# Kernel optimization log

Measured on AMD Instinct MI355X. Metric: run time of the kernel, lower is better.

## Reference

```python
import jax, jax.numpy as jnp
import numpy as np

B, T, C = 512, 256, 384
HEAD_SIZE = 64

def setup_inputs() -> dict:
    key = jax.random.key(0)
    k1, k2, k3, k4 = jax.random.split(key, 4)
    x = jax.random.normal(k1, (B, T, C), dtype=jnp.float32)
    # nn.Linear(n_embed, head_size, bias=False) weights, stored as [C, head_size] for x @ W
    s = 1.0 / np.sqrt(C)
    Wk = jax.random.uniform(k2, (C, HEAD_SIZE), dtype=jnp.float32, minval=-s, maxval=s)
    Wq = jax.random.uniform(k3, (C, HEAD_SIZE), dtype=jnp.float32, minval=-s, maxval=s)
    Wv = jax.random.uniform(k4, (C, HEAD_SIZE), dtype=jnp.float32, minval=-s, maxval=s)
    return {"x": x, "Wk": Wk, "Wq": Wq, "Wv": Wv}

def reference(x, Wk, Wq, Wv):
    # Single causal self-attention head (eval mode: dropout is identity).
    Bx, Tx, Cx = x.shape
    k = jnp.einsum('btc,ch->bth', x, Wk)   # [B,T,H]
    q = jnp.einsum('btc,ch->bth', x, Wq)
    v = jnp.einsum('btc,ch->bth', x, Wv)
    # NOTE: original scales by C**-0.5 with C = input embed dim (384), not head_size.
    wei = jnp.einsum('bth,bsh->bts', q, k) * (Cx ** -0.5)  # [B,T,T]
    causal = jnp.tril(jnp.ones((Tx, Tx), dtype=bool))
    wei = jnp.where(causal, wei, -jnp.inf)
    wei = jax.nn.softmax(wei, axis=-1)
    out = jnp.einsum('bts,bsh->bth', wei, v)  # [B,T,H]
    return out
```

## Files before the change

kernel.cpp:

```cpp
#include <hip/hip_runtime.h>

typedef __attribute__((ext_vector_type(4))) float f32x4;
typedef __attribute__((ext_vector_type(8))) short short8;
typedef unsigned int u32;
typedef unsigned long long u64;
typedef unsigned short u16;

#define NB 512
#define TT 256
#define CC 384
#define HH 64

__device__ __forceinline__ u16 fbf(float f) {
    u32 u = __builtin_bit_cast(u32, f);
    u32 r = u + 0x7fffu + ((u >> 16) & 1u);
    return (u16)(r >> 16);
}

__device__ __forceinline__ f32x4 mfma16x16x32(short8 a, short8 b, f32x4 c) {
    return __builtin_amdgcn_mfma_f32_16x16x32_bf16(a, b, c, 0, 0, 0);
}

__global__ __launch_bounds__(256) void prep_w(const float* __restrict__ Wk,
                                              const float* __restrict__ Wq,
                                              const float* __restrict__ Wv,
                                              u16* __restrict__ WbT) {
    int t = blockIdx.x * 256 + threadIdx.x;
    if (t >= 144 * 64) return;
    int lane = t & 63;
    int fi = t >> 6;
    int mat = fi / 48;
    int kt = (fi >> 2) % 12;
    int nt = fi & 3;
    const float* W = (mat == 0) ? Wq : (mat == 1 ? Wk : Wv);
    float scale = (mat == 0) ? 0.05103103630798288f : 1.0f;
    int c0 = 32 * kt + 8 * (lane >> 4);
    int h = 16 * nt + (lane & 15);
#pragma unroll
    for (int j = 0; j < 8; ++j)
        WbT[(size_t)t * 8 + j] = fbf(W[(c0 + j) * HH + h] * scale);
}

__global__ __launch_bounds__(512) void attn_head(const float* __restrict__ x,
                                                 const u16* __restrict__ WbT,
                                                 float* __restrict__ out) {
    __shared__ __align__(16) u16 Klds[TT * HH];
    __shared__ __align__(16) u16 Vtlds[HH * TT];
    __shared__ __align__(16) u16 Pscr[8 * 32 * 64];

    const int tid = (int)threadIdx.x;
    const int lane = tid & 63;
    const int w = tid >> 6;
    const int c = lane & 15;
    const int g = lane >> 4;
    const int b = (int)blockIdx.x;
    const int m0 = 32 * w;

    char* kbase = (char*)Klds;
    char* vbase = (char*)Vtlds;
    char* sbase = (char*)(Pscr + w * 2048);

    f32x4 acc[3][2][4];
#pragma unroll
    for (int m = 0; m < 3; ++m)
#pragma unroll
        for (int tm = 0; tm < 2; ++tm)
#pragma unroll
            for (int nt = 0; nt < 4; ++nt)
                acc[m][tm][nt] = (f32x4){0.f, 0.f, 0.f, 0.f};

    const float* xb = x + (size_t)b * TT * CC;

    for (int kt = 0; kt < 12; ++kt) {
        short8 afr[2];
#pragma unroll
        for (int tm = 0; tm < 2; ++tm) {
            const float* p = xb + (size_t)(m0 + 16 * tm + c) * CC + 32 * kt + 8 * g;
            f32x4 f0 = *(const f32x4*)p;
            f32x4 f1 = *(const f32x4*)(p + 4);
            short8 a;
            a[0] = (short)fbf(f0[0]); a[1] = (short)fbf(f0[1]);
            a[2] = (short)fbf(f0[2]); a[3] = (short)fbf(f0[3]);
            a[4] = (short)fbf(f1[0]); a[5] = (short)fbf(f1[1]);
            a[6] = (short)fbf(f1[2]); a[7] = (short)fbf(f1[3]);
            afr[tm] = a;
        }
#pragma unroll
        for (int mat = 0; mat < 3; ++mat) {
#pragma unroll
            for (int nt = 0; nt < 4; ++nt) {
                short8 bfr = *(const short8*)(WbT + (size_t)(((mat * 12 + kt) * 4 + nt) * 64 + lane) * 8);
                acc[mat][0][nt] = mfma16x16x32(afr[0], bfr, acc[mat][0][nt]);
                acc[mat][1][nt] = mfma16x16x32(afr[1], bfr, acc[mat][1][nt]);
            }
        }
    }

#pragma unroll
    for (int tm = 0; tm < 2; ++tm)
#pragma unroll
        for (int nt = 0; nt < 4; ++nt)
#pragma unroll
            for (int r = 0; r < 4; ++r) {
                int q = 16 * tm + 4 * g + r;
                int hh = 16 * nt + c;
                *(u16*)(sbase + q * 128 + ((hh * 2) ^ ((q & 7) << 4))) = fbf(acc[0][tm][nt][r]);
            }
    short8 Qf[2][2];
#pragma unroll
    for (int tm = 0; tm < 2; ++tm)
#pragma unroll
        for (int kt = 0; kt < 2; ++kt) {
            int q = 16 * tm + c;
            Qf[tm][kt] = *(const short8*)(sbase + q * 128 + ((64 * kt + 16 * g) ^ ((q & 7) << 4)));
        }

#pragma unroll
    for (int tm = 0; tm < 2; ++tm)
#pragma unroll
        for (int nt = 0; nt < 4; ++nt) {
            int hh = 16 * nt + c;
#pragma unroll
            for (int r = 0; r < 4; ++r) {
                int s = m0 + 16 * tm + 4 * g + r;
                *(u16*)(kbase + s * 128 + ((hh * 2) ^ ((s & 7) << 4))) = fbf(acc[1][tm][nt][r]);
            }
            int sb4 = m0 + 16 * tm + 4 * g;
            u64 pk = (u64)fbf(acc[2][tm][nt][0]) | ((u64)fbf(acc[2][tm][nt][1]) << 16) |
                     ((u64)fbf(acc[2][tm][nt][2]) << 32) | ((u64)fbf(acc[2][tm][nt][3]) << 48);
            *(u64*)(vbase + hh * 512 + ((sb4 * 2) ^ ((hh & 7) << 4))) = pk;
        }

    __syncthreads();

    float m_run0 = -1e30f, m_run1 = -1e30f, l_run0 = 0.f, l_run1 = 0.f;
    f32x4 o[2][4];
#pragma unroll
    for (int tm = 0; tm < 2; ++tm)
#pragma unroll
        for (int ht = 0; ht < 4; ++ht)
            o[tm][ht] = (f32x4){0.f, 0.f, 0.f, 0.f};

    const int nch = (w >> 1) + 1;
    for (int ci = 0; ci < nch; ++ci) {
        const int s0 = 64 * ci;
        int stmax = (m0 + 31 - s0) >> 4;
        stmax = stmax > 3 ? 3 : stmax;

        f32x4 SS[4][2];
#pragma unroll
        for (int st = 0; st < 4; ++st) {
            SS[st][0] = (f32x4){0.f, 0.f, 0.f, 0.f};
            SS[st][1] = (f32x4){0.f, 0.f, 0.f, 0.f};
        }
#pragma unroll
        for (int kt = 0; kt < 2; ++kt) {
#pragma unroll
            for (int st = 0; st < 4; ++st) {
                if (st <= stmax) {
                    int s = s0 + 16 * st + c;
                    short8 kf = *(const short8*)(kbase + s * 128 + ((64 * kt + 16 * g) ^ ((s & 7) << 4)));
                    SS[st][0] = mfma16x16x32(kf, Qf[0][kt], SS[st][0]);
                    SS[st][1] = mfma16x16x32(kf, Qf[1][kt], SS[st][1]);
                }
            }
        }

        float mx0 = -1e30f, mx1 = -1e30f;
        const int qg0 = m0 + c, qg1 = m0 + 16 + c;
#pragma unroll
        for (int st = 0; st < 4; ++st) {
            if (st > stmax) continue;
#pragma unroll
            for (int r = 0; r < 4; ++r) {
                int sg = s0 + 16 * st + 4 * g + r;
                float v0 = SS[st][0][r], v1 = SS[st][1][r];
                v0 = (sg > qg0) ? -1e30f : v0;
                v1 = (sg > qg1) ? -1e30f : v1;
                SS[st][0][r] = v0; SS[st][1][r] = v1;
                mx0 = fmaxf(mx0, v0); mx1 = fmaxf(mx1, v1);
            }
        }
        mx0 = fmaxf(mx0, __shfl_xor(mx0, 16));
        mx0 = fmaxf(mx0, __shfl_xor(mx0, 32));
        mx1 = fmaxf(mx1, __shfl_xor(mx1, 16));
        mx1 = fmaxf(mx1, __shfl_xor(mx1, 32));

        float mn0 = fmaxf(m_run0, mx0), mn1 = fmaxf(m_run1, mx1);
        float fs0 = __expf(m_run0 - mn0), fs1 = __expf(m_run1 - mn1);
        m_run0 = mn0; m_run1 = mn1;

        float ls0 = 0.f, ls1 = 0.f;
#pragma unroll
        for (int st = 0; st < 4; ++st) {
            if (st > stmax) continue;
#pragma unroll
            for (int r = 0; r < 4; ++r) {
                float p0 = __expf(SS[st][0][r] - mn0);
                float p1 = __expf(SS[st][1][r] - mn1);
                SS[st][0][r] = p0; SS[st][1][r] = p1;
                ls0 += p0; ls1 += p1;
            }
        }
        ls0 += __shfl_xor(ls0, 16); ls0 += __shfl_xor(ls0, 32);
        ls1 += __shfl_xor(ls1, 16); ls1 += __shfl_xor(ls1, 32);
        l_run0 = l_run0 * fs0 + ls0;
        l_run1 = l_run1 * fs1 + ls1;

#pragma unroll
        for (int r = 0; r < 4; ++r) {
            float fr0 = __shfl(fs0, (g << 2) + r);
            float fr1 = __shfl(fs1, (g << 2) + r);
#pragma unroll
            for (int ht = 0; ht < 4; ++ht) {
                o[0][ht][r] *= fr0;
                o[1][ht][r] *= fr1;
            }
        }

#pragma unroll
        for (int st = 0; st < 4; ++st) {
            if (st > stmax) continue;
#pragma unroll
            for (int tm = 0; tm < 2; ++tm) {
                int ql = 16 * tm + c;
                u32 lo = (u32)fbf(SS[st][tm][0]) | ((u32)fbf(SS[st][tm][1]) << 16);
                u32 hi = (u32)fbf(SS[st][tm][2]) | ((u32)fbf(SS[st][tm][3]) << 16);
                *(u64*)(sbase + ql * 128 + ((32 * st + 8 * g) ^ ((ql & 7) << 4))) = (u64)lo | ((u64)hi << 32);
            }
        }

        const int ksmax = stmax >> 1;
#pragma unroll
        for (int ks = 0; ks < 2; ++ks) {
            if (ks > ksmax) continue;
            short8 Pf0 = *(const short8*)(sbase + c * 128 + ((64 * ks + 16 * g) ^ ((c & 7) << 4)));
            short8 Pf1 = *(const short8*)(sbase + (16 + c) * 128 + ((64 * ks + 16 * g) ^ ((c & 7) << 4)));
#pragma unroll
            for (int ht = 0; ht < 4; ++ht) {
                int hh = 16 * ht + c;
                short8 vf = *(const short8*)(vbase + hh * 512 + ((2 * s0 + 64 * ks + 16 * g) ^ ((hh & 7) << 4)));
                o[0][ht] = mfma16x16x32(Pf0, vf, o[0][ht]);
                o[1][ht] = mfma16x16x32(Pf1, vf, o[1][ht]);
            }
        }
    }

    float* ob = out + ((size_t)b * TT + m0) * HH;
    float ri0 = 1.f / l_run0, ri1 = 1.f / l_run1;
#pragma unroll
    for (int r = 0; r < 4; ++r) {
        float rr0 = __shfl(ri0, (g << 2) + r);
        float rr1 = __shfl(ri1, (g << 2) + r);
#pragma unroll
        for (int ht = 0; ht < 4; ++ht) {
            ob[(4 * g + r) * HH + 16 * ht + c] = o[0][ht][r] * rr0;
            ob[(16 + 4 * g + r) * HH + 16 * ht + c] = o[1][ht][r] * rr1;
        }
    }
}

extern "C" void kernel_launch(void* const* d_in, const int* in_sizes, int n_in,
                              void* d_out, int out_size, void* d_ws, size_t ws_size,
                              hipStream_t stream) {
    (void)in_sizes; (void)n_in; (void)out_size; (void)ws_size;
    const float* x = (const float*)d_in[0];
    const float* Wk = (const float*)d_in[1];
    const float* Wq = (const float*)d_in[2];
    const float* Wv = (const float*)d_in[3];
    u16* WbT = (u16*)d_ws;
    float* out = (float*)d_out;

    prep_w<<<36, 256, 0, stream>>>(Wk, Wq, Wv, WbT);
    attn_head<<<NB, 512, 0, stream>>>(x, WbT, out);
}
```

Measured before the change: 72.96 us.

## Balance causal work across waves and pass P through shuffles instead of LDS

Each wave now owns two 16-row query tiles from opposite ends of the sequence (16w and 240-16w), so the causal attention work is the same for every wave instead of growing with wave index. The per-wave P scratch buffer in LDS is removed. Q is staged through the K buffer, and the softmax probabilities are rearranged into MFMA operand layout with cross-lane shuffles. Float-to-bf16 packing now uses the v_cvt_pk_bf16_f32 instruction, and launch bounds request 4 blocks per CU, which adds register pressure and more shuffle instructions.

Result: slower. 175.2 us (+140.1%).

```diff
diff --git a/kernel.cpp b/kernel.cpp
--- a/kernel.cpp
+++ b/kernel.cpp
@@ -1,6 +1,7 @@
 #include <hip/hip_runtime.h>
 
 typedef __attribute__((ext_vector_type(4))) float f32x4;
+typedef __attribute__((ext_vector_type(4))) int i32x4;
 typedef __attribute__((ext_vector_type(8))) short short8;
 typedef unsigned int u32;
 typedef unsigned long long u64;
@@ -15,6 +16,12 @@
     u32 u = __builtin_bit_cast(u32, f);
     u32 r = u + 0x7fffu + ((u >> 16) & 1u);
     return (u16)(r >> 16);
+}
+
+__device__ __forceinline__ u32 cvtpk(float lo, float hi) {
+    u32 r;
+    asm("v_cvt_pk_bf16_f32 %0, %1, %2" : "=v"(r) : "v"(lo), "v"(hi));
+    return r;
 }
 
 __device__ __forceinline__ f32x4 mfma16x16x32(short8 a, short8 b, f32x4 c) {
@@ -41,12 +48,11 @@
         WbT[(size_t)t * 8 + j] = fbf(W[(c0 + j) * HH + h] * scale);
 }
 
-__global__ __launch_bounds__(512) void attn_head(const float* __restrict__ x,
-                                                 const u16* __restrict__ WbT,
-                                                 float* __restrict__ out) {
+__global__ __launch_bounds__(512, 4) void attn_head(const float* __restrict__ x,
+                                                    const u16* __restrict__ WbT,
+                                                    float* __restrict__ out) {
     __shared__ __align__(16) u16 Klds[TT * HH];
     __shared__ __align__(16) u16 Vtlds[HH * TT];
-    __shared__ __align__(16) u16 Pscr[8 * 32 * 64];
 
     const int tid = (int)threadIdx.x;
     const int lane = tid & 63;
@@ -54,208 +60,251 @@
     const int c = lane & 15;
     const int g = lane >> 4;
     const int b = (int)blockIdx.x;
-    const int m0 = 32 * w;
+    const int grow0 = 16 * w;
+    const int grow1 = 240 - 16 * w;
 
     char* kbase = (char*)Klds;
     char* vbase = (char*)Vtlds;
-    char* sbase = (char*)(Pscr + w * 2048);
-
-    f32x4 acc[3][2][4];
-#pragma unroll
-    for (int m = 0; m < 3; ++m)
-#pragma unroll
-        for (int tm = 0; tm < 2; ++tm)
+    const float* xb = x + (size_t)b * TT * CC;
+
+    short8 Qf[2][2];
+
+#pragma unroll
+    for (int tm = 0; tm < 2; ++tm) {
+        const int gr = (tm == 0) ? grow0 : grow1;
+        f32x4 acc[3][4];
+#pragma unroll
+        for (int m = 0; m < 3; ++m)
 #pragma unroll
             for (int nt = 0; nt < 4; ++nt)
-                acc[m][tm][nt] = (f32x4){0.f, 0.f, 0.f, 0.f};
-
-    const float* xb = x + (size_t)b * TT * CC;
-
-    for (int kt = 0; kt < 12; ++kt) {
-        short8 afr[2];
-#pragma unroll
-        for (int tm = 0; tm < 2; ++tm) {
-            const float* p = xb + (size_t)(m0 + 16 * tm + c) * CC + 32 * kt + 8 * g;
+                acc[m][nt] = (f32x4){0.f, 0.f, 0.f, 0.f};
+
+        for (int kt = 0; kt < 12; ++kt) {
+            const float* p = xb + (size_t)(gr + c) * CC + 32 * kt + 8 * g;
             f32x4 f0 = *(const f32x4*)p;
             f32x4 f1 = *(const f32x4*)(p + 4);
-            short8 a;
-            a[0] = (short)fbf(f0[0]); a[1] = (short)fbf(f0[1]);
-            a[2] = (short)fbf(f0[2]); a[3] = (short)fbf(f0[3]);
-            a[4] = (short)fbf(f1[0]); a[5] = (short)fbf(f1[1]);
-            a[6] = (short)fbf(f1[2]); a[7] = (short)fbf(f1[3]);
-            afr[tm] = a;
-        }
-#pragma unroll
-        for (int mat = 0; mat < 3; ++mat) {
-#pragma unroll
-            for (int nt = 0; nt < 4; ++nt) {
-                short8 bfr = *(const short8*)(WbT + (size_t)(((mat * 12 + kt) * 4 + nt) * 64 + lane) * 8);
-                acc[mat][0][nt] = mfma16x16x32(afr[0], bfr, acc[mat][0][nt]);
-                acc[mat][1][nt] = mfma16x16x32(afr[1], bfr, acc[mat][1][nt]);
-            }
-        }
-    }
-
-#pragma unroll
-    for (int tm = 0; tm < 2; ++tm)
+            i32x4 aw = {(int)cvtpk(f0[0], f0[1]), (int)cvtpk(f0[2], f0[3]),
+                        (int)cvtpk(f1[0], f1[1]), (int)cvtpk(f1[2], f1[3])};
+            short8 afr = __builtin_bit_cast(short8, aw);
+#pragma unroll
+            for (int mat = 0; mat < 3; ++mat)
+#pragma unroll
+                for (int nt = 0; nt < 4; ++nt) {
+                    short8 bfr = *(const short8*)(WbT + (size_t)(((mat * 12 + kt) * 4 + nt) * 64 + lane) * 8);
+                    acc[mat][nt] = mfma16x16x32(afr, bfr, acc[mat][nt]);
+                }
+        }
+
 #pragma unroll
         for (int nt = 0; nt < 4; ++nt)
 #pragma unroll
             for (int r = 0; r < 4; ++r) {
-                int q = 16 * tm + 4 * g + r;
+                int q = gr + 4 * g + r;
                 int hh = 16 * nt + c;
-                *(u16*)(sbase + q * 128 + ((hh * 2) ^ ((q & 7) << 4))) = fbf(acc[0][tm][nt][r]);
-            }
-    short8 Qf[2][2];
-#pragma unroll
-    for (int tm = 0; tm < 2; ++tm)
+                *(u16*)(kbase + q * 128 + ((hh * 2) ^ ((q & 7) << 4))) = fbf(acc[0][nt][r]);
+            }
 #pragma unroll
         for (int kt = 0; kt < 2; ++kt) {
-            int q = 16 * tm + c;
-            Qf[tm][kt] = *(const short8*)(sbase + q * 128 + ((64 * kt + 16 * g) ^ ((q & 7) << 4)));
-        }
-
-#pragma unroll
-    for (int tm = 0; tm < 2; ++tm)
+            int q = gr + c;
+            Qf[tm][kt] = *(const short8*)(kbase + q * 128 + ((64 * kt + 16 * g) ^ ((q & 7) << 4)));
+        }
+
 #pragma unroll
         for (int nt = 0; nt < 4; ++nt) {
             int hh = 16 * nt + c;
 #pragma unroll
             for (int r = 0; r < 4; ++r) {
-                int s = m0 + 16 * tm + 4 * g + r;
-                *(u16*)(kbase + s * 128 + ((hh * 2) ^ ((s & 7) << 4))) = fbf(acc[1][tm][nt][r]);
-            }
-            int sb4 = m0 + 16 * tm + 4 * g;
-            u64 pk = (u64)fbf(acc[2][tm][nt][0]) | ((u64)fbf(acc[2][tm][nt][1]) << 16) |
-                     ((u64)fbf(acc[2][tm][nt][2]) << 32) | ((u64)fbf(acc[2][tm][nt][3]) << 48);
-            *(u64*)(vbase + hh * 512 + ((sb4 * 2) ^ ((hh & 7) << 4))) = pk;
-        }
+                int s = gr + 4 * g + r;
+                *(u16*)(kbase + s * 128 + ((hh * 2) ^ ((s & 7) << 4))) = fbf(acc[1][nt][r]);
+            }
+            int sb4 = gr + 4 * g;
+            u64 pkv = (u64)cvtpk(acc[2][nt][0], acc[2][nt][1]) |
+                      ((u64)cvtpk(acc[2][nt][2], acc[2][nt][3]) << 32);
+            *(u64*)(vbase + hh * 512 + ((sb4 * 2) ^ ((hh & 7) << 4))) = pkv;
+        }
+    }
 
     __syncthreads();
 
     float m_run0 = -1e30f, m_run1 = -1e30f, l_run0 = 0.f, l_run1 = 0.f;
-    f32x4 o[2][4];
-#pragma unroll
-    for (int tm = 0; tm < 2; ++tm)
-#pragma unroll
-        for (int ht = 0; ht < 4; ++ht)
-            o[tm][ht] = (f32x4){0.f, 0.f, 0.f, 0.f};
-
-    const int nch = (w >> 1) + 1;
-    for (int ci = 0; ci < nch; ++ci) {
+    f32x4 o0[4], o1[4];
+#pragma unroll
+    for (int ht = 0; ht < 4; ++ht) {
+        o0[ht] = (f32x4){0.f, 0.f, 0.f, 0.f};
+        o1[ht] = (f32x4){0.f, 0.f, 0.f, 0.f};
+    }
+
+    const int lastc0 = (grow0 + 15) >> 6;
+    const int lastc1 = (grow1 + 15) >> 6;
+    const int srcLo = c + ((lane & 16) << 1);
+    const int srcHi = srcLo + 16;
+    const bool hiHalf = (lane >= 32);
+
+    for (int ci = 0; ci <= lastc1; ++ci) {
         const int s0 = 64 * ci;
-        int stmax = (m0 + 31 - s0) >> 4;
-        stmax = stmax > 3 ? 3 : stmax;
-
-        f32x4 SS[4][2];
+        const bool act0 = (ci <= lastc0);
+        const int stmax0 = act0 ? min(3, (grow0 + 15 - s0) >> 4) : -1;
+        const int stmax1 = min(3, (grow1 + 15 - s0) >> 4);
+        const int stmaxU = max(stmax0, stmax1);
+
+        f32x4 SS0[4], SS1[4];
 #pragma unroll
         for (int st = 0; st < 4; ++st) {
-            SS[st][0] = (f32x4){0.f, 0.f, 0.f, 0.f};
-            SS[st][1] = (f32x4){0.f, 0.f, 0.f, 0.f};
+            SS0[st] = (f32x4){0.f, 0.f, 0.f, 0.f};
+            SS1[st] = (f32x4){0.f, 0.f, 0.f, 0.f};
         }
 #pragma unroll
         for (int kt = 0; kt < 2; ++kt) {
 #pragma unroll
             for (int st = 0; st < 4; ++st) {
-                if (st <= stmax) {
+                if (st <= stmaxU) {
                     int s = s0 + 16 * st + c;
                     short8 kf = *(const short8*)(kbase + s * 128 + ((64 * kt + 16 * g) ^ ((s & 7) << 4)));
-                    SS[st][0] = mfma16x16x32(kf, Qf[0][kt], SS[st][0]);
-                    SS[st][1] = mfma16x16x32(kf, Qf[1][kt], SS[st][1]);
+                    if (st <= stmax0) SS0[st] = mfma16x16x32(kf, Qf[0][kt], SS0[st]);
+                    if (st <= stmax1) SS1[st] = mfma16x16x32(kf, Qf[1][kt], SS1[st]);
                 }
             }
         }
 
         float mx0 = -1e30f, mx1 = -1e30f;
-        const int qg0 = m0 + c, qg1 = m0 + 16 + c;
+        const int qg0 = grow0 + c, qg1 = grow1 + c;
 #pragma unroll
         for (int st = 0; st < 4; ++st) {
-            if (st > stmax) continue;
 #pragma unroll
             for (int r = 0; r < 4; ++r) {
                 int sg = s0 + 16 * st + 4 * g + r;
-                float v0 = SS[st][0][r], v1 = SS[st][1][r];
-                v0 = (sg > qg0) ? -1e30f : v0;
-                v1 = (sg > qg1) ? -1e30f : v1;
-                SS[st][0][r] = v0; SS[st][1][r] = v1;
-                mx0 = fmaxf(mx0, v0); mx1 = fmaxf(mx1, v1);
-            }
-        }
-        mx0 = fmaxf(mx0, __shfl_xor(mx0, 16));
-        mx0 = fmaxf(mx0, __shfl_xor(mx0, 32));
+                if (st <= stmax0) {
+                    float v = (sg > qg0) ? -1e30f : SS0[st][r];
+                    SS0[st][r] = v;
+                    mx0 = fmaxf(mx0, v);
+                }
+                if (st <= stmax1) {
+                    float v = (sg > qg1) ? -1e30f : SS1[st][r];
+                    SS1[st][r] = v;
+                    mx1 = fmaxf(mx1, v);
+                }
+            }
+        }
+        if (act0) {
+            mx0 = fmaxf(mx0, __shfl_xor(mx0, 16));
+            mx0 = fmaxf(mx0, __shfl_xor(mx0, 32));
+        }
         mx1 = fmaxf(mx1, __shfl_xor(mx1, 16));
         mx1 = fmaxf(mx1, __shfl_xor(mx1, 32));
 
-        float mn0 = fmaxf(m_run0, mx0), mn1 = fmaxf(m_run1, mx1);
-        float fs0 = __expf(m_run0 - mn0), fs1 = __expf(m_run1 - mn1);
-        m_run0 = mn0; m_run1 = mn1;
+        float fs0 = 1.f, fs1;
+        if (act0) {
+            float mn0 = fmaxf(m_run0, mx0);
+            fs0 = __expf(m_run0 - mn0);
+            m_run0 = mn0;
+        }
+        {
+            float mn1 = fmaxf(m_run1, mx1);
+            fs1 = __expf(m_run1 - mn1);
+            m_run1 = mn1;
+        }
 
         float ls0 = 0.f, ls1 = 0.f;
 #pragma unroll
         for (int st = 0; st < 4; ++st) {
-            if (st > stmax) continue;
 #pragma unroll
             for (int r = 0; r < 4; ++r) {
-                float p0 = __expf(SS[st][0][r] - mn0);
-                float p1 = __expf(SS[st][1][r] - mn1);
-                SS[st][0][r] = p0; SS[st][1][r] = p1;
-                ls0 += p0; ls1 += p1;
-            }
-        }
-        ls0 += __shfl_xor(ls0, 16); ls0 += __shfl_xor(ls0, 32);
-        ls1 += __shfl_xor(ls1, 16); ls1 += __shfl_xor(ls1, 32);
-        l_run0 = l_run0 * fs0 + ls0;
+                if (st <= stmax0) {
+                    float p = __expf(SS0[st][r] - m_run0);
+                    SS0[st][r] = p;
+                    ls0 += p;
+                }
+                if (st <= stmax1) {
+                    float p = __expf(SS1[st][r] - m_run1);
+                    SS1[st][r] = p;
+                    ls1 += p;
+                }
+            }
+        }
+        if (act0) {
+            ls0 += __shfl_xor(ls0, 16);
+            ls0 += __shfl_xor(ls0, 32);
+            l_run0 = l_run0 * fs0 + ls0;
+        }
+        ls1 += __shfl_xor(ls1, 16);
+        ls1 += __shfl_xor(ls1, 32);
         l_run1 = l_run1 * fs1 + ls1;
 
 #pragma unroll
         for (int r = 0; r < 4; ++r) {
-            float fr0 = __shfl(fs0, (g << 2) + r);
-            float fr1 = __shfl(fs1, (g << 2) + r);
+            float fr0 = __shfl(fs0, 4 * g + r);
+            float fr1 = __shfl(fs1, 4 * g + r);
 #pragma unroll
             for (int ht = 0; ht < 4; ++ht) {
-                o[0][ht][r] *= fr0;
-                o[1][ht][r] *= fr1;
-            }
-        }
-
+                if (act0) o0[ht][r] *= fr0;
+                o1[ht][r] *= fr1;
+            }
+        }
+
+        u32 pk0[4][2], pk1[4][2];
 #pragma unroll
         for (int st = 0; st < 4; ++st) {
-            if (st > stmax) continue;
-#pragma unroll
-            for (int tm = 0; tm < 2; ++tm) {
-                int ql = 16 * tm + c;
-                u32 lo = (u32)fbf(SS[st][tm][0]) | ((u32)fbf(SS[st][tm][1]) << 16);
-                u32 hi = (u32)fbf(SS[st][tm][2]) | ((u32)fbf(SS[st][tm][3]) << 16);
-                *(u64*)(sbase + ql * 128 + ((32 * st + 8 * g) ^ ((ql & 7) << 4))) = (u64)lo | ((u64)hi << 32);
-            }
-        }
-
-        const int ksmax = stmax >> 1;
+            pk0[st][0] = cvtpk(SS0[st][0], SS0[st][1]);
+            pk0[st][1] = cvtpk(SS0[st][2], SS0[st][3]);
+            pk1[st][0] = cvtpk(SS1[st][0], SS1[st][1]);
+            pk1[st][1] = cvtpk(SS1[st][2], SS1[st][3]);
+        }
+
+        const int ksmax0 = stmax0 >> 1;
+        const int ksmax1 = stmax1 >> 1;
 #pragma unroll
         for (int ks = 0; ks < 2; ++ks) {
-            if (ks > ksmax) continue;
-            short8 Pf0 = *(const short8*)(sbase + c * 128 + ((64 * ks + 16 * g) ^ ((c & 7) << 4)));
-            short8 Pf1 = *(const short8*)(sbase + (16 + c) * 128 + ((64 * ks + 16 * g) ^ ((c & 7) << 4)));
+            const bool u0 = (ks <= ksmax0);
+            const bool u1 = (ks <= ksmax1);
+            if (!(u0 || u1)) continue;
+            short8 Pf0, Pf1;
+            if (u0) {
+                u32 a0 = (u32)__shfl((int)pk0[2 * ks][0], srcLo);
+                u32 b0 = (u32)__shfl((int)pk0[2 * ks + 1][0], srcLo);
+                u32 a1 = (u32)__shfl((int)pk0[2 * ks][1], srcLo);
+                u32 b1 = (u32)__shfl((int)pk0[2 * ks + 1][1], srcLo);
+                u32 a2 = (u32)__shfl((int)pk0[2 * ks][0], srcHi);
+                u32 b2 = (u32)__shfl((int)pk0[2 * ks + 1][0], srcHi);
+                u32 a3 = (u32)__shfl((int)pk0[2 * ks][1], srcHi);
+                u32 b3 = (u32)__shfl((int)pk0[2 * ks + 1][1], srcHi);
+                i32x4 t = {(int)(hiHalf ? b0 : a0), (int)(hiHalf ? b1 : a1),
+                           (int)(hiHalf ? b2 : a2), (int)(hiHalf ? b3 : a3)};
+                Pf0 = __builtin_bit_cast(short8, t);
+            }
+            if (u1) {
+                u32 a0 = (u32)__shfl((int)pk1[2 * ks][0], srcLo);
+                u32 b0 = (u32)__shfl((int)pk1[2 * ks + 1][0], srcLo);
+                u32 a1 = (u32)__shfl((int)pk1[2 * ks][1], srcLo);
+                u32 b1 = (u32)__shfl((int)pk1[2 * ks + 1][1], srcLo);
+                u32 a2 = (u32)__shfl((int)pk1[2 * ks][0], srcHi);
+                u32 b2 = (u32)__shfl((int)pk1[2 * ks + 1][0], srcHi);
+                u32 a3 = (u32)__shfl((int)pk1[2 * ks][1], srcHi);
+                u32 b3 = (u32)__shfl((int)pk1[2 * ks + 1][1], srcHi);
+                i32x4 t = {(int)(hiHalf ? b0 : a0), (int)(hiHalf ? b1 : a1),
+                           (int)(hiHalf ? b2 : a2), (int)(hiHalf ? b3 : a3)};
+                Pf1 = __builtin_bit_cast(short8, t);
+            }
 #pragma unroll
             for (int ht = 0; ht < 4; ++ht) {
                 int hh = 16 * ht + c;
                 short8 vf = *(const short8*)(vbase + hh * 512 + ((2 * s0 + 64 * ks + 16 * g) ^ ((hh & 7) << 4)));
-                o[0][ht] = mfma16x16x32(Pf0, vf, o[0][ht]);
-                o[1][ht] = mfma16x16x32(Pf1, vf, o[1][ht]);
+                if (u0) o0[ht] = mfma16x16x32(Pf0, vf, o0[ht]);
+                if (u1) o1[ht] = mfma16x16x32(Pf1, vf, o1[ht]);
             }
         }
     }
 
-    float* ob = out + ((size_t)b * TT + m0) * HH;
     float ri0 = 1.f / l_run0, ri1 = 1.f / l_run1;
+    float* ob0 = out + ((size_t)b * TT + grow0) * HH;
+    float* ob1 = out + ((size_t)b * TT + grow1) * HH;
 #pragma unroll
     for (int r = 0; r < 4; ++r) {
-        float rr0 = __shfl(ri0, (g << 2) + r);
-        float rr1 = __shfl(ri1, (g << 2) + r);
+        float rr0 = __shfl(ri0, 4 * g + r);
+        float rr1 = __shfl(ri1, 4 * g + r);
 #pragma unroll
         for (int ht = 0; ht < 4; ++ht) {
-            ob[(4 * g + r) * HH + 16 * ht + c] = o[0][ht][r] * rr0;
-            ob[(16 + 4 * g + r) * HH + 16 * ht + c] = o[1][ht][r] * rr1;
+            ob0[(4 * g + r) * HH + 16 * ht + c] = o0[ht][r] * rr0;
+            ob1[(4 * g + r) * HH + 16 * ht + c] = o1[ht][r] * rr1;
         }
     }
 }
```

## Balance causal work across waves with paired row tiles and hardware bf16 packing

Applied to the files above, without the earlier changes.

Each wave now owns two 16-row query tiles taken from opposite ends of the sequence (16w and 240-16w), so every wave does about the same amount of causal attention work. Before, waves owning later rows did far more chunks than waves owning early rows. The projection and attention loops now handle one tile at a time, which lowers register pressure; launch bounds ask for 4 blocks per CU. Other changes: Q is staged through K's LDS slot before K overwrites it, the scratch buffer is halved, and fp32-to-bf16 conversion uses v_cvt_pk_bf16_f32. Masking is skipped for chunks that need none, and the first-chunk rescale is skipped.

New measurement: 129.2 us. +77.1%, slower.

```diff
diff --git a/kernel.cpp b/kernel.cpp
--- a/kernel.cpp
+++ b/kernel.cpp
@@ -1,6 +1,7 @@
 #include <hip/hip_runtime.h>
 
 typedef __attribute__((ext_vector_type(4))) float f32x4;
+typedef __attribute__((ext_vector_type(4))) int i32x4;
 typedef __attribute__((ext_vector_type(8))) short short8;
 typedef unsigned int u32;
 typedef unsigned long long u64;
@@ -15,6 +16,12 @@
     u32 u = __builtin_bit_cast(u32, f);
     u32 r = u + 0x7fffu + ((u >> 16) & 1u);
     return (u16)(r >> 16);
+}
+
+__device__ __forceinline__ u32 cvtpk(float lo, float hi) {
+    u32 r;
+    asm("v_cvt_pk_bf16_f32 %0, %1, %2" : "=v"(r) : "v"(lo), "v"(hi));
+    return r;
 }
 
 __device__ __forceinline__ f32x4 mfma16x16x32(short8 a, short8 b, f32x4 c) {
@@ -41,12 +48,12 @@
         WbT[(size_t)t * 8 + j] = fbf(W[(c0 + j) * HH + h] * scale);
 }
 
-__global__ __launch_bounds__(512) void attn_head(const float* __restrict__ x,
-                                                 const u16* __restrict__ WbT,
-                                                 float* __restrict__ out) {
+__global__ __launch_bounds__(512, 4) void attn_head(const float* __restrict__ x,
+                                                    const u16* __restrict__ WbT,
+                                                    float* __restrict__ out) {
     __shared__ __align__(16) u16 Klds[TT * HH];
     __shared__ __align__(16) u16 Vtlds[HH * TT];
-    __shared__ __align__(16) u16 Pscr[8 * 32 * 64];
+    __shared__ __align__(16) u16 Pscr[8 * 16 * 64];
 
     const int tid = (int)threadIdx.x;
     const int lane = tid & 63;
@@ -54,208 +61,182 @@
     const int c = lane & 15;
     const int g = lane >> 4;
     const int b = (int)blockIdx.x;
-    const int m0 = 32 * w;
 
     char* kbase = (char*)Klds;
     char* vbase = (char*)Vtlds;
-    char* sbase = (char*)(Pscr + w * 2048);
-
-    f32x4 acc[3][2][4];
-#pragma unroll
-    for (int m = 0; m < 3; ++m)
-#pragma unroll
-        for (int tm = 0; tm < 2; ++tm)
+    char* sbase = (char*)(Pscr + w * 1024);
+    const float* xb = x + (size_t)b * TT * CC;
+
+    short8 Qf[2][2];
+
+#pragma unroll
+    for (int tm = 0; tm < 2; ++tm) {
+        const int gr = (tm == 0) ? 16 * w : 240 - 16 * w;
+        f32x4 acc[3][4];
+#pragma unroll
+        for (int m = 0; m < 3; ++m)
 #pragma unroll
             for (int nt = 0; nt < 4; ++nt)
-                acc[m][tm][nt] = (f32x4){0.f, 0.f, 0.f, 0.f};
-
-    const float* xb = x + (size_t)b * TT * CC;
-
-    for (int kt = 0; kt < 12; ++kt) {
-        short8 afr[2];
-#pragma unroll
-        for (int tm = 0; tm < 2; ++tm) {
-            const float* p = xb + (size_t)(m0 + 16 * tm + c) * CC + 32 * kt + 8 * g;
-            f32x4 f0 = *(const f32x4*)p;
-            f32x4 f1 = *(const f32x4*)(p + 4);
-            short8 a;
-            a[0] = (short)fbf(f0[0]); a[1] = (short)fbf(f0[1]);
-            a[2] = (short)fbf(f0[2]); a[3] = (short)fbf(f0[3]);
-            a[4] = (short)fbf(f1[0]); a[5] = (short)fbf(f1[1]);
-            a[6] = (short)fbf(f1[2]); a[7] = (short)fbf(f1[3]);
-            afr[tm] = a;
-        }
-#pragma unroll
-        for (int mat = 0; mat < 3; ++mat) {
-#pragma unroll
-            for (int nt = 0; nt < 4; ++nt) {
-                short8 bfr = *(const short8*)(WbT + (size_t)(((mat * 12 + kt) * 4 + nt) * 64 + lane) * 8);
-                acc[mat][0][nt] = mfma16x16x32(afr[0], bfr, acc[mat][0][nt]);
-                acc[mat][1][nt] = mfma16x16x32(afr[1], bfr, acc[mat][1][nt]);
+                acc[m][nt] = (f32x4){0.f, 0.f, 0.f, 0.f};
+
+        const float* prow = xb + (size_t)(gr + c) * CC + 8 * g;
+#pragma unroll
+        for (int kt = 0; kt < 12; ++kt) {
+            f32x4 f0 = *(const f32x4*)(prow + 32 * kt);
+            f32x4 f1 = *(const f32x4*)(prow + 32 * kt + 4);
+            i32x4 aw = {(int)cvtpk(f0[0], f0[1]), (int)cvtpk(f0[2], f0[3]),
+                        (int)cvtpk(f1[0], f1[1]), (int)cvtpk(f1[2], f1[3])};
+            short8 afr = __builtin_bit_cast(short8, aw);
+#pragma unroll
+            for (int mat = 0; mat < 3; ++mat)
+#pragma unroll
+                for (int nt = 0; nt < 4; ++nt) {
+                    short8 bfr = *(const short8*)(WbT + (size_t)(((mat * 12 + kt) * 4 + nt) * 64 + lane) * 8);
+                    acc[mat][nt] = mfma16x16x32(afr, bfr, acc[mat][nt]);
+                }
+        }
+
+#pragma unroll
+        for (int nt = 0; nt < 4; ++nt)
+#pragma unroll
+            for (int r = 0; r < 4; ++r) {
+                int q = gr + 4 * g + r;
+                int hh = 16 * nt + c;
+                *(u16*)(kbase + q * 128 + ((hh * 2) ^ ((q & 7) << 4))) = fbf(acc[0][nt][r]);
             }
-        }
-    }
-
-#pragma unroll
-    for (int tm = 0; tm < 2; ++tm)
-#pragma unroll
-        for (int nt = 0; nt < 4; ++nt)
-#pragma unroll
-            for (int r = 0; r < 4; ++r) {
-                int q = 16 * tm + 4 * g + r;
-                int hh = 16 * nt + c;
-                *(u16*)(sbase + q * 128 + ((hh * 2) ^ ((q & 7) << 4))) = fbf(acc[0][tm][nt][r]);
-            }
-    short8 Qf[2][2];
-#pragma unroll
-    for (int tm = 0; tm < 2; ++tm)
 #pragma unroll
         for (int kt = 0; kt < 2; ++kt) {
-            int q = 16 * tm + c;
-            Qf[tm][kt] = *(const short8*)(sbase + q * 128 + ((64 * kt + 16 * g) ^ ((q & 7) << 4)));
-        }
-
-#pragma unroll
-    for (int tm = 0; tm < 2; ++tm)
+            int q = gr + c;
+            Qf[tm][kt] = *(const short8*)(kbase + q * 128 + ((64 * kt + 16 * g) ^ ((q & 7) << 4)));
+        }
+
 #pragma unroll
         for (int nt = 0; nt < 4; ++nt) {
             int hh = 16 * nt + c;
 #pragma unroll
             for (int r = 0; r < 4; ++r) {
-                int s = m0 + 16 * tm + 4 * g + r;
-                *(u16*)(kbase + s * 128 + ((hh * 2) ^ ((s & 7) << 4))) = fbf(acc[1][tm][nt][r]);
+                int s = gr + 4 * g + r;
+                *(u16*)(kbase + s * 128 + ((hh * 2) ^ ((s & 7) << 4))) = fbf(acc[1][nt][r]);
             }
-            int sb4 = m0 + 16 * tm + 4 * g;
-            u64 pk = (u64)fbf(acc[2][tm][nt][0]) | ((u64)fbf(acc[2][tm][nt][1]) << 16) |
-                     ((u64)fbf(acc[2][tm][nt][2]) << 32) | ((u64)fbf(acc[2][tm][nt][3]) << 48);
-            *(u64*)(vbase + hh * 512 + ((sb4 * 2) ^ ((hh & 7) << 4))) = pk;
-        }
+            int sb4 = gr + 4 * g;
+            u64 pkv = (u64)cvtpk(acc[2][nt][0], acc[2][nt][1]) |
+                      ((u64)cvtpk(acc[2][nt][2], acc[2][nt][3]) << 32);
+            *(u64*)(vbase + hh * 512 + ((sb4 * 2) ^ ((hh & 7) << 4))) = pkv;
+        }
+    }
 
     __syncthreads();
 
-    float m_run0 = -1e30f, m_run1 = -1e30f, l_run0 = 0.f, l_run1 = 0.f;
-    f32x4 o[2][4];
-#pragma unroll
-    for (int tm = 0; tm < 2; ++tm)
+#pragma unroll
+    for (int tm = 0; tm < 2; ++tm) {
+        const int gr = (tm == 0) ? 16 * w : 240 - 16 * w;
+        const int lastc = (gr + 15) >> 6;
+        const int qg = gr + c;
+
+        float m_run = -1e30f, l_run = 0.f;
+        f32x4 o[4];
 #pragma unroll
         for (int ht = 0; ht < 4; ++ht)
-            o[tm][ht] = (f32x4){0.f, 0.f, 0.f, 0.f};
-
-    const int nch = (w >> 1) + 1;
-    for (int ci = 0; ci < nch; ++ci) {
-        const int s0 = 64 * ci;
-        int stmax = (m0 + 31 - s0) >> 4;
-        stmax = stmax > 3 ? 3 : stmax;
-
-        f32x4 SS[4][2];
-#pragma unroll
-        for (int st = 0; st < 4; ++st) {
-            SS[st][0] = (f32x4){0.f, 0.f, 0.f, 0.f};
-            SS[st][1] = (f32x4){0.f, 0.f, 0.f, 0.f};
-        }
-#pragma unroll
-        for (int kt = 0; kt < 2; ++kt) {
-#pragma unroll
-            for (int st = 0; st < 4; ++st) {
-                if (st <= stmax) {
-                    int s = s0 + 16 * st + c;
-                    short8 kf = *(const short8*)(kbase + s * 128 + ((64 * kt + 16 * g) ^ ((s & 7) << 4)));
-                    SS[st][0] = mfma16x16x32(kf, Qf[0][kt], SS[st][0]);
-                    SS[st][1] = mfma16x16x32(kf, Qf[1][kt], SS[st][1]);
+            o[ht] = (f32x4){0.f, 0.f, 0.f, 0.f};
+
+        for (int ci = 0; ci <= lastc; ++ci) {
+            const int s0 = 64 * ci;
+            int stx = (gr + 15 - s0) >> 4;
+            const int stmax = stx > 3 ? 3 : stx;
+            const bool needMask = (s0 + 63 > gr);
+
+            f32x4 SS[4];
+#pragma unroll
+            for (int st = 0; st < 4; ++st)
+                SS[st] = (f32x4){0.f, 0.f, 0.f, 0.f};
+#pragma unroll
+            for (int kt = 0; kt < 2; ++kt)
+#pragma unroll
+                for (int st = 0; st < 4; ++st)
+                    if (st <= stmax) {
+                        int s = s0 + 16 * st + c;
+                        short8 kf = *(const short8*)(kbase + s * 128 + ((64 * kt + 16 * g) ^ ((s & 7) << 4)));
+                        SS[st] = mfma16x16x32(kf, Qf[tm][kt], SS[st]);
+                    }
+
+            float mx = -1e30f;
+#pragma unroll
+            for (int st = 0; st < 4; ++st)
+                if (st <= stmax)
+#pragma unroll
+                    for (int r = 0; r < 4; ++r) {
+                        float v = SS[st][r];
+                        if (needMask) {
+                            int sg = s0 + 16 * st + 4 * g + r;
+                            v = (sg > qg) ? -1e30f : v;
+                            SS[st][r] = v;
+                        }
+                        mx = fmaxf(mx, v);
+                    }
+            mx = fmaxf(mx, __shfl_xor(mx, 16));
+            mx = fmaxf(mx, __shfl_xor(mx, 32));
+
+            float mn = fmaxf(m_run, mx);
+            float fs = __expf(m_run - mn);
+            m_run = mn;
+
+            float ls = 0.f;
+#pragma unroll
+            for (int st = 0; st < 4; ++st)
+                if (st <= stmax)
+#pragma unroll
+                    for (int r = 0; r < 4; ++r) {
+                        float p = __expf(SS[st][r] - mn);
+                        SS[st][r] = p;
+                        ls += p;
+                    }
+            ls += __shfl_xor(ls, 16);
+            ls += __shfl_xor(ls, 32);
+            l_run = l_run * fs + ls;
+
+            if (ci) {
+#pragma unroll
+                for (int r = 0; r < 4; ++r) {
+                    float fr = __shfl(fs, 4 * g + r);
+#pragma unroll
+                    for (int ht = 0; ht < 4; ++ht)
+                        o[ht][r] *= fr;
                 }
             }
-        }
-
-        float mx0 = -1e30f, mx1 = -1e30f;
-        const int qg0 = m0 + c, qg1 = m0 + 16 + c;
-#pragma unroll
-        for (int st = 0; st < 4; ++st) {
-            if (st > stmax) continue;
-#pragma unroll
-            for (int r = 0; r < 4; ++r) {
-                int sg = s0 + 16 * st + 4 * g + r;
-                float v0 = SS[st][0][r], v1 = SS[st][1][r];
-                v0 = (sg > qg0) ? -1e30f : v0;
-                v1 = (sg > qg1) ? -1e30f : v1;
-                SS[st][0][r] = v0; SS[st][1][r] = v1;
-                mx0 = fmaxf(mx0, v0); mx1 = fmaxf(mx1, v1);
-            }
-        }
-        mx0 = fmaxf(mx0, __shfl_xor(mx0, 16));
-        mx0 = fmaxf(mx0, __shfl_xor(mx0, 32));
-        mx1 = fmaxf(mx1, __shfl_xor(mx1, 16));
-        mx1 = fmaxf(mx1, __shfl_xor(mx1, 32));
-
-        float mn0 = fmaxf(m_run0, mx0), mn1 = fmaxf(m_run1, mx1);
-        float fs0 = __expf(m_run0 - mn0), fs1 = __expf(m_run1 - mn1);
-        m_run0 = mn0; m_run1 = mn1;
-
-        float ls0 = 0.f, ls1 = 0.f;
-#pragma unroll
-        for (int st = 0; st < 4; ++st) {
-            if (st > stmax) continue;
-#pragma unroll
-            for (int r = 0; r < 4; ++r) {
-                float p0 = __expf(SS[st][0][r] - mn0);
-                float p1 = __expf(SS[st][1][r] - mn1);
-                SS[st][0][r] = p0; SS[st][1][r] = p1;
-                ls0 += p0; ls1 += p1;
-            }
-        }
-        ls0 += __shfl_xor(ls0, 16); ls0 += __shfl_xor(ls0, 32);
-        ls1 += __shfl_xor(ls1, 16); ls1 += __shfl_xor(ls1, 32);
-        l_run0 = l_run0 * fs0 + ls0;
-        l_run1 = l_run1 * fs1 + ls1;
-
+
+            const int stW = stmax | 1;
+#pragma unroll
+            for (int st = 0; st < 4; ++st)
+                if (st <= stW) {
+                    u64 pp = 0;
+                    if (st <= stmax)
+                        pp = (u64)cvtpk(SS[st][0], SS[st][1]) |
+                             ((u64)cvtpk(SS[st][2], SS[st][3]) << 32);
+                    *(u64*)(sbase + c * 128 + ((32 * st + 8 * g) ^ ((c & 7) << 4))) = pp;
+                }
+
+            const int ksmax = stmax >> 1;
+#pragma unroll
+            for (int ks = 0; ks < 2; ++ks)
+                if (ks <= ksmax) {
+                    short8 Pf = *(const short8*)(sbase + c * 128 + ((64 * ks + 16 * g) ^ ((c & 7) << 4)));
+#pragma unroll
+                    for (int ht = 0; ht < 4; ++ht) {
+                        int hh = 16 * ht + c;
+                        short8 vf = *(const short8*)(vbase + hh * 512 + ((2 * s0 + 64 * ks + 16 * g) ^ ((hh & 7) << 4)));
+                        o[ht] = mfma16x16x32(Pf, vf, o[ht]);
+                    }
+                }
+        }
+
+        float ri = 1.f / l_run;
+        float* ob = out + ((size_t)b * TT + gr) * HH;
 #pragma unroll
         for (int r = 0; r < 4; ++r) {
-            float fr0 = __shfl(fs0, (g << 2) + r);
-            float fr1 = __shfl(fs1, (g << 2) + r);
-#pragma unroll
-            for (int ht = 0; ht < 4; ++ht) {
-                o[0][ht][r] *= fr0;
-                o[1][ht][r] *= fr1;
-            }
-        }
-
-#pragma unroll
-        for (int st = 0; st < 4; ++st) {
-            if (st > stmax) continue;
-#pragma unroll
-            for (int tm = 0; tm < 2; ++tm) {
-                int ql = 16 * tm + c;
-                u32 lo = (u32)fbf(SS[st][tm][0]) | ((u32)fbf(SS[st][tm][1]) << 16);
-                u32 hi = (u32)fbf(SS[st][tm][2]) | ((u32)fbf(SS[st][tm][3]) << 16);
-                *(u64*)(sbase + ql * 128 + ((32 * st + 8 * g) ^ ((ql & 7) << 4))) = (u64)lo | ((u64)hi << 32);
-            }
-        }
-
-        const int ksmax = stmax >> 1;
-#pragma unroll
-        for (int ks = 0; ks < 2; ++ks) {
-            if (ks > ksmax) continue;
-            short8 Pf0 = *(const short8*)(sbase + c * 128 + ((64 * ks + 16 * g) ^ ((c & 7) << 4)));
-            short8 Pf1 = *(const short8*)(sbase + (16 + c) * 128 + ((64 * ks + 16 * g) ^ ((c & 7) << 4)));
-#pragma unroll
-            for (int ht = 0; ht < 4; ++ht) {
-                int hh = 16 * ht + c;
-                short8 vf = *(const short8*)(vbase + hh * 512 + ((2 * s0 + 64 * ks + 16 * g) ^ ((hh & 7) << 4)));
-                o[0][ht] = mfma16x16x32(Pf0, vf, o[0][ht]);
-                o[1][ht] = mfma16x16x32(Pf1, vf, o[1][ht]);
-            }
-        }
-    }
-
-    float* ob = out + ((size_t)b * TT + m0) * HH;
-    float ri0 = 1.f / l_run0, ri1 = 1.f / l_run1;
-#pragma unroll
-    for (int r = 0; r < 4; ++r) {
-        float rr0 = __shfl(ri0, (g << 2) + r);
-        float rr1 = __shfl(ri1, (g << 2) + r);
-#pragma unroll
-        for (int ht = 0; ht < 4; ++ht) {
-            ob[(4 * g + r) * HH + 16 * ht + c] = o[0][ht][r] * rr0;
-            ob[(16 + 4 * g + r) * HH + 16 * ht + c] = o[1][ht][r] * rr1;
+            float rr = __shfl(ri, 4 * g + r);
+#pragma unroll
+            for (int ht = 0; ht < 4; ++ht)
+                ob[(4 * g + r) * HH + 16 * ht + c] = o[ht][r] * rr;
         }
     }
 }
```
